# Kernel optimization log

Hardware: AMD Instinct MI355X
Metric: run time of the kernel (lower is better)

The kernel has to match this reference:

```python
import jax, jax.numpy as jnp
import numpy as np

B = 64          # number of scenes/graphs
OBJS = 2048     # objects per scene
N = B * OBJS    # total objects
D = 256         # representation_dim
K = 2           # num_channels


def setup_inputs() -> dict:
    key = jax.random.key(0)
    k1, k2, k3 = jax.random.split(key, 3)
    x_aggregation = jax.random.normal(k1, (N, D), dtype=jnp.float32)
    num_objs = jnp.full((B,), OBJS, dtype=jnp.int32)
    # glorot for att_shared [1, D]: fan_in + fan_out = 1 + D
    std_shared = float(np.sqrt(6.0 / (1 + D)))
    att_shared = jax.random.uniform(k2, (1, D), dtype=jnp.float32,
                                    minval=-std_shared, maxval=std_shared)
    # glorot for att_scale [K, 1]
    std_scale = float(np.sqrt(6.0 / (K + 1)))
    att_scale = jax.random.uniform(k3, (K, 1), dtype=jnp.float32,
                                   minval=-std_scale, maxval=std_scale)
    channel_bias = jnp.zeros((K, D), dtype=jnp.float32)
    return {"x_aggregation": x_aggregation, "num_objs": num_objs,
            "att_shared": att_shared, "att_scale": att_scale,
            "channel_bias": channel_bias}


def reference(x_aggregation, num_objs, att_shared, att_scale, channel_bias):
    batch_idx = jnp.repeat(jnp.arange(B), num_objs, total_repeat_length=N)  # [N]
    # scatter_mean: per-scene context features [B, D]
    seg_sum = jax.ops.segment_sum(x_aggregation, batch_idx, num_segments=B)
    counts = jnp.maximum(num_objs, 1).astype(x_aggregation.dtype)
    ctx = seg_sum / counts[:, None]
    attn_in = jax.nn.leaky_relu(x_aggregation + ctx[batch_idx], negative_slope=0.2)  # [N, D]
    # per-channel logits: ((attn_in + bias[k]) . att_shared) * scale[k]
    base = attn_in @ att_shared[0]                 # [N]
    bias_term = channel_bias @ att_shared[0]       # [K]
    logits = (base[:, None] + bias_term[None, :]) * att_scale[:, 0][None, :]  # [N, K]
    # per-channel segment softmax over objects within each scene
    m = jax.ops.segment_max(logits, batch_idx, num_segments=B)   # [B, K]
    z = jnp.exp(logits - m[batch_idx])
    s = jax.ops.segment_sum(z, batch_idx, num_segments=B)        # [B, K]
    attn_weights = z / s[batch_idx]                              # [N, K]
    # attention-weighted pooling per channel -> [B, D, K]
    weighted = x_aggregation[:, :, None] * attn_weights[:, None, :]  # [N, D, K]
    scene_features = jax.ops.segment_sum(weighted, batch_idx, num_segments=B)
    return scene_features, attn_weights
```

## Files before the change

### kernel.cpp

```cpp
#include <hip/hip_runtime.h>

#define B    64
#define OBJS 2048
#define NTOT (B * OBJS)
#define D    256
#define K    2
#define S1   16
#define CH   (OBJS / S1)
#define RPW  (CH / 4)

#define WS_P1  0
#define WS_UP  (1024 * 256)
#define WS_ZP  (WS_UP + 1024 * 512)
#define WS_E   (WS_ZP + 1024 * 8)

static __device__ __forceinline__ float lrelu02(float v) {
    return v > 0.0f ? v : 0.2f * v;
}

__global__ __launch_bounds__(256) void k1_partial(const float* __restrict__ x,
                                                  float* __restrict__ ws) {
    __shared__ float red[4 * D];
    int blk = blockIdx.x;
    int w = threadIdx.x >> 6, l = threadIdx.x & 63;
    int row0 = blk * CH + w * RPW;

    float4 acc = make_float4(0.f, 0.f, 0.f, 0.f);
    const float* px = x + (size_t)row0 * D + 4 * l;
#pragma unroll 8
    for (int j = 0; j < RPW; ++j) {
        float4 v = *(const float4*)(px + (size_t)j * D);
        acc.x += v.x; acc.y += v.y; acc.z += v.z; acc.w += v.w;
    }
    *(float4*)(red + w * D + 4 * l) = acc;
    __syncthreads();
    int t = threadIdx.x;
    if (t < 64) {
        float4 a = ((const float4*)(red        ))[t];
        float4 e = ((const float4*)(red +     D))[t];
        float4 f = ((const float4*)(red + 2 * D))[t];
        float4 g = ((const float4*)(red + 3 * D))[t];
        float4 s = make_float4(a.x + e.x + f.x + g.x, a.y + e.y + f.y + g.y,
                               a.z + e.z + f.z + g.z, a.w + e.w + f.w + g.w);
        *(float4*)(ws + WS_P1 + blk * D + 4 * t) = s;
    }
}

__global__ __launch_bounds__(256) void k2_main(const float* __restrict__ x,
                                               const int* __restrict__ num_objs,
                                               const float* __restrict__ att_scale,
                                               const float* __restrict__ att_shared,
                                               const float* __restrict__ channel_bias,
                                               float* __restrict__ ws) {
    __shared__ float pl[4 * 576];
    __shared__ float esm[4 * 16];
    __shared__ float sctx[D];
    __shared__ float sbt[2];

    int blk = blockIdx.x;
    int b = blk >> 4;
    int t = threadIdx.x;
    int w = t >> 6, l = t & 63;
    int r = l & 7, s = l >> 3;
    int row0 = blk * CH + w * RPW;

    {
        int cnt = num_objs[b]; if (cnt < 1) cnt = 1;
        float inv = 1.0f / (float)cnt;
        float sum = 0.f;
#pragma unroll
        for (int c = 0; c < S1; ++c) sum += ws[WS_P1 + (b * S1 + c) * D + t];
        sctx[t] = sum * inv;
    }
    if (t < 64) {
        float4 a = ((const float4*)att_shared)[t];
#pragma unroll
        for (int k = 0; k < K; ++k) {
            float4 cb = ((const float4*)(channel_bias + k * D))[t];
            float v = a.x * cb.x + a.y * cb.y + a.z * cb.z + a.w * cb.w;
#pragma unroll
            for (int m = 32; m > 0; m >>= 1) v += __shfl_xor(v, m);
            if (t == 0) sbt[k] = v;
        }
    }
    __syncthreads();

    float4 a4   = ((const float4*)att_shared)[l];
    float4 ctx4 = *(const float4*)(sctx + 4 * l);
    float bt0 = sbt[0], bt1 = sbt[1];
    float s0 = att_scale[0], s1 = att_scale[1];

    float4 acc0 = make_float4(0.f, 0.f, 0.f, 0.f);
    float4 acc1 = make_float4(0.f, 0.f, 0.f, 0.f);
    float z0 = 0.f, z1 = 0.f;
    float e0c = 0.f, e1c = 0.f;
    float* pw = pl  + w * 576;
    float* ew = esm + w * 16;
    const float* px = x + (size_t)row0 * D + 4 * l;

#pragma unroll
    for (int g = 0; g < 4; ++g) {
        float4 v0 = *(const float4*)(px + (size_t)(g * 8 + 0) * D);
        float4 v1 = *(const float4*)(px + (size_t)(g * 8 + 1) * D);
        float4 v2 = *(const float4*)(px + (size_t)(g * 8 + 2) * D);
        float4 v3 = *(const float4*)(px + (size_t)(g * 8 + 3) * D);
        float4 v4 = *(const float4*)(px + (size_t)(g * 8 + 4) * D);
        float4 v5 = *(const float4*)(px + (size_t)(g * 8 + 5) * D);
        float4 v6 = *(const float4*)(px + (size_t)(g * 8 + 6) * D);
        float4 v7 = *(const float4*)(px + (size_t)(g * 8 + 7) * D);

#define PDOT(V) (lrelu02((V).x + ctx4.x) * a4.x + lrelu02((V).y + ctx4.y) * a4.y \
               + lrelu02((V).z + ctx4.z) * a4.z + lrelu02((V).w + ctx4.w) * a4.w)
        pw[l * 9 + 0] = PDOT(v0); pw[l * 9 + 1] = PDOT(v1);
        pw[l * 9 + 2] = PDOT(v2); pw[l * 9 + 3] = PDOT(v3);
        pw[l * 9 + 4] = PDOT(v4); pw[l * 9 + 5] = PDOT(v5);
        pw[l * 9 + 6] = PDOT(v6); pw[l * 9 + 7] = PDOT(v7);
#undef PDOT
        float tr = 0.f;
#pragma unroll
        for (int q = 0; q < 8; ++q) tr += pw[(s * 8 + q) * 9 + r];
        tr += __shfl_xor(tr, 8);
        tr += __shfl_xor(tr, 16);
        tr += __shfl_xor(tr, 32);

        float e0 = __expf((tr + bt0) * s0);
        float e1 = __expf((tr + bt1) * s1);
        if (((l >> 3) & 3) == g) { e0c = e0; e1c = e1; }
        if (l < 8) { ew[2 * l] = e0; ew[2 * l + 1] = e1; }
        float4 E0 = *(const float4*)(ew + 0);
        float4 E1 = *(const float4*)(ew + 4);
        float4 E2 = *(const float4*)(ew + 8);
        float4 E3 = *(const float4*)(ew + 12);
        z0 += E0.x + E0.z + E1.x + E1.z + E2.x + E2.z + E3.x + E3.z;
        z1 += E0.y + E0.w + E1.y + E1.w + E2.y + E2.w + E3.y + E3.w;

#define ACC(V, EA, EB) { acc0.x += (V).x * (EA); acc0.y += (V).y * (EA);      \
                         acc0.z += (V).z * (EA); acc0.w += (V).w * (EA);      \
                         acc1.x += (V).x * (EB); acc1.y += (V).y * (EB);      \
                         acc1.z += (V).z * (EB); acc1.w += (V).w * (EB); }
        ACC(v0, E0.x, E0.y) ACC(v1, E0.z, E0.w)
        ACC(v2, E1.x, E1.y) ACC(v3, E1.z, E1.w)
        ACC(v4, E2.x, E2.y) ACC(v5, E2.z, E2.w)
        ACC(v6, E3.x, E3.y) ACC(v7, E3.z, E3.w)
#undef ACC
    }

    if (l < 32) ((float2*)(ws + WS_E))[row0 + l] = make_float2(e0c, e1c);
    if (l == 0) {
        ws[WS_ZP + blk * 8 + w * 2 + 0] = z0;
        ws[WS_ZP + blk * 8 + w * 2 + 1] = z1;
    }
    __syncthreads();
    {
        int base = w * (D * K) + l * 8;
        pl[base + 0] = acc0.x; pl[base + 1] = acc1.x;
        pl[base + 2] = acc0.y; pl[base + 3] = acc1.y;
        pl[base + 4] = acc0.z; pl[base + 5] = acc1.z;
        pl[base + 6] = acc0.w; pl[base + 7] = acc1.w;
    }
    __syncthreads();
    if (t < 128) {
        float4 a = ((const float4*)(pl       ))[t];
        float4 e = ((const float4*)(pl +  512))[t];
        float4 f = ((const float4*)(pl + 1024))[t];
        float4 g = ((const float4*)(pl + 1536))[t];
        float4 s4 = make_float4(a.x + e.x + f.x + g.x, a.y + e.y + f.y + g.y,
                                a.z + e.z + f.z + g.z, a.w + e.w + f.w + g.w);
        *(float4*)(ws + WS_UP + (size_t)blk * (D * K) + 4 * t) = s4;
    }
}

__global__ __launch_bounds__(256) void k3_final(const float* __restrict__ ws,
                                                float* __restrict__ out) {
    __shared__ float zsh[2];
    int b = blockIdx.x;
    int t = threadIdx.x;
    int w = t >> 6, l = t & 63;

    if (w < 2) {
        float v = ws[WS_ZP + (b * S1 + (l >> 2)) * 8 + (l & 3) * 2 + w];
#pragma unroll
        for (int m = 32; m > 0; m >>= 1) v += __shfl_xor(v, m);
        if (l == 0) zsh[w] = v;
    }
    __syncthreads();
    float z0 = zsh[0], z1 = zsh[1];
    float iz0 = 1.0f / z0, iz1 = 1.0f / z1;

#pragma unroll
    for (int j = t; j < D * K; j += 256) {
        float s = 0.f;
#pragma unroll
        for (int c = 0; c < S1; ++c) s += ws[WS_UP + (b * S1 + c) * (D * K) + j];
        out[b * (D * K) + j] = s * ((j & 1) ? iz1 : iz0);
    }
    const float4* E = (const float4*)(ws + WS_E);
    float4* W = (float4*)(out + B * D * K);
#pragma unroll
    for (int i = t; i < OBJS / 2; i += 256) {
        float4 e = E[b * (OBJS / 2) + i];
        W[b * (OBJS / 2) + i] = make_float4(e.x * iz0, e.y * iz1, e.z * iz0, e.w * iz1);
    }
}

extern "C" void kernel_launch(void* const* d_in, const int* in_sizes, int n_in,
                              void* d_out, int out_size, void* d_ws, size_t ws_size,
                              hipStream_t stream) {
    const float* x            = (const float*)d_in[0];
    const int*   num_objs     = (const int*)d_in[1];
    const float* att_shared   = (const float*)d_in[2];
    const float* att_scale    = (const float*)d_in[3];
    const float* channel_bias = (const float*)d_in[4];
    float* ws  = (float*)d_ws;
    float* out = (float*)d_out;

    k1_partial<<<B * S1, 256, 0, stream>>>(x, ws);
    k2_main<<<B * S1, 256, 0, stream>>>(x, num_objs, att_scale, att_shared,
                                        channel_bias, ws);
    k3_final<<<B, 256, 0, stream>>>(ws, out);
}
```

Measured before the change: 222.7 us.

## Fuse three kernels into one using per-scene atomic barriers

Merges the partial-sum, main and final kernels into one launch. Blocks of a scene meet at an atomic counter barrier to share the context mean, and the last block to arrive does the final normalisation. This removes two kernel launches and the gaps between them, and the second read of x may now hit in cache. In exchange it adds a memset launch and relies on all 16 blocks of a scene being co-resident, which makes the spin-wait a deadlock risk guarded only by an iteration cap.

```diff
diff --git a/kernel.cpp b/kernel.cpp
--- a/kernel.cpp
+++ b/kernel.cpp
@@ -5,57 +5,40 @@
 #define NTOT (B * OBJS)
 #define D    256
 #define K    2
-#define S1   16
-#define CH   (OBJS / S1)
+#define SPB  16
+#define GRID (B * SPB)
+#define CH   (OBJS / SPB)
 #define RPW  (CH / 4)
 
+
 #define WS_P1  0
-#define WS_UP  (1024 * 256)
-#define WS_ZP  (WS_UP + 1024 * 512)
-#define WS_E   (WS_ZP + 1024 * 8)
+#define WS_UP  (GRID * 256)
+#define WS_ZP  (WS_UP + GRID * 512)
+#define WS_E   (WS_ZP + GRID * 8)
+#define WS_CNT (WS_E + NTOT * 2)
 
 static __device__ __forceinline__ float lrelu02(float v) {
     return v > 0.0f ? v : 0.2f * v;
 }
 
-__global__ __launch_bounds__(256) void k1_partial(const float* __restrict__ x,
-                                                  float* __restrict__ ws) {
-    __shared__ float red[4 * D];
-    int blk = blockIdx.x;
-    int w = threadIdx.x >> 6, l = threadIdx.x & 63;
-    int row0 = blk * CH + w * RPW;
-
-    float4 acc = make_float4(0.f, 0.f, 0.f, 0.f);
-    const float* px = x + (size_t)row0 * D + 4 * l;
-#pragma unroll 8
-    for (int j = 0; j < RPW; ++j) {
-        float4 v = *(const float4*)(px + (size_t)j * D);
-        acc.x += v.x; acc.y += v.y; acc.z += v.z; acc.w += v.w;
-    }
-    *(float4*)(red + w * D + 4 * l) = acc;
-    __syncthreads();
-    int t = threadIdx.x;
-    if (t < 64) {
-        float4 a = ((const float4*)(red        ))[t];
-        float4 e = ((const float4*)(red +     D))[t];
-        float4 f = ((const float4*)(red + 2 * D))[t];
-        float4 g = ((const float4*)(red + 3 * D))[t];
-        float4 s = make_float4(a.x + e.x + f.x + g.x, a.y + e.y + f.y + g.y,
-                               a.z + e.z + f.z + g.z, a.w + e.w + f.w + g.w);
-        *(float4*)(ws + WS_P1 + blk * D + 4 * t) = s;
-    }
-}
-
-__global__ __launch_bounds__(256) void k2_main(const float* __restrict__ x,
-                                               const int* __restrict__ num_objs,
-                                               const float* __restrict__ att_scale,
-                                               const float* __restrict__ att_shared,
-                                               const float* __restrict__ channel_bias,
-                                               float* __restrict__ ws) {
+static __device__ __forceinline__ float ldg_agent(const float* p) {
+    return __hip_atomic_load(p, __ATOMIC_RELAXED, __HIP_MEMORY_SCOPE_AGENT);
+}
+
+__global__ __launch_bounds__(256, 4)
+void fused_kernel(const float* __restrict__ x,
+                  const int* __restrict__ num_objs,
+                  const float* __restrict__ att_scale,
+                  const float* __restrict__ att_shared,
+                  const float* __restrict__ channel_bias,
+                  float* __restrict__ ws,
+                  float* __restrict__ out) {
     __shared__ float pl[4 * 576];
     __shared__ float esm[4 * 16];
     __shared__ float sctx[D];
     __shared__ float sbt[2];
+    __shared__ int   sarr;
+    __shared__ float zsh[2];
 
     int blk = blockIdx.x;
     int b = blk >> 4;
@@ -63,25 +46,62 @@
     int w = t >> 6, l = t & 63;
     int r = l & 7, s = l >> 3;
     int row0 = blk * CH + w * RPW;
+    int* cnt1 = (int*)(ws + WS_CNT) + b;
+    int* cnt2 = (int*)(ws + WS_CNT) + 64 + b;
+
+    {
+        float4 acc = make_float4(0.f, 0.f, 0.f, 0.f);
+        const float* px = x + (size_t)row0 * D + 4 * l;
+#pragma unroll 8
+        for (int j = 0; j < RPW; ++j) {
+            float4 v = *(const float4*)(px + (size_t)j * D);
+            acc.x += v.x; acc.y += v.y; acc.z += v.z; acc.w += v.w;
+        }
+        *(float4*)(pl + w * D + 4 * l) = acc;
+    }
+    __syncthreads();
+    if (t < 64) {
+        float4 a = ((const float4*)(pl        ))[t];
+        float4 e = ((const float4*)(pl +     D))[t];
+        float4 f = ((const float4*)(pl + 2 * D))[t];
+        float4 g = ((const float4*)(pl + 3 * D))[t];
+        float4 sm = make_float4(a.x + e.x + f.x + g.x, a.y + e.y + f.y + g.y,
+                                a.z + e.z + f.z + g.z, a.w + e.w + f.w + g.w);
+        *(float4*)(ws + WS_P1 + (size_t)blk * D + 4 * t) = sm;
+    }
+    if (w == 1) {
+        float4 a = ((const float4*)att_shared)[l];
+#pragma unroll
+        for (int k = 0; k < K; ++k) {
+            float4 cb = ((const float4*)(channel_bias + k * D))[l];
+            float v = a.x * cb.x + a.y * cb.y + a.z * cb.z + a.w * cb.w;
+#pragma unroll
+            for (int m = 32; m > 0; m >>= 1) v += __shfl_xor(v, m);
+            if (l == 0) { sbt[0 + k] = v; }
+        }
+    }
+
+    __builtin_amdgcn_fence(__ATOMIC_RELEASE, "agent");
+    __syncthreads();
+    if (t == 0) {
+        __hip_atomic_fetch_add(cnt1, 1, __ATOMIC_ACQ_REL, __HIP_MEMORY_SCOPE_AGENT);
+        int it = 0;
+        while (__hip_atomic_load(cnt1, __ATOMIC_ACQUIRE, __HIP_MEMORY_SCOPE_AGENT) < SPB) {
+            __builtin_amdgcn_s_sleep(2);
+            if (++it > (1 << 24)) break;
+        }
+    }
+    __syncthreads();
+    __builtin_amdgcn_fence(__ATOMIC_ACQUIRE, "agent");
 
     {
         int cnt = num_objs[b]; if (cnt < 1) cnt = 1;
         float inv = 1.0f / (float)cnt;
         float sum = 0.f;
 #pragma unroll
-        for (int c = 0; c < S1; ++c) sum += ws[WS_P1 + (b * S1 + c) * D + t];
+        for (int c = 0; c < SPB; ++c)
+            sum += ldg_agent(&ws[WS_P1 + (size_t)(b * SPB + c) * D + t]);
         sctx[t] = sum * inv;
-    }
-    if (t < 64) {
-        float4 a = ((const float4*)att_shared)[t];
-#pragma unroll
-        for (int k = 0; k < K; ++k) {
-            float4 cb = ((const float4*)(channel_bias + k * D))[t];
-            float v = a.x * cb.x + a.y * cb.y + a.z * cb.z + a.w * cb.w;
-#pragma unroll
-            for (int m = 32; m > 0; m >>= 1) v += __shfl_xor(v, m);
-            if (t == 0) sbt[k] = v;
-        }
     }
     __syncthreads();
 
@@ -168,38 +188,39 @@
                                 a.z + e.z + f.z + g.z, a.w + e.w + f.w + g.w);
         *(float4*)(ws + WS_UP + (size_t)blk * (D * K) + 4 * t) = s4;
     }
-}
-
-__global__ __launch_bounds__(256) void k3_final(const float* __restrict__ ws,
-                                                float* __restrict__ out) {
-    __shared__ float zsh[2];
-    int b = blockIdx.x;
-    int t = threadIdx.x;
-    int w = t >> 6, l = t & 63;
+
+    __builtin_amdgcn_fence(__ATOMIC_RELEASE, "agent");
+    __syncthreads();
+    if (t == 0)
+        sarr = __hip_atomic_fetch_add(cnt2, 1, __ATOMIC_ACQ_REL, __HIP_MEMORY_SCOPE_AGENT);
+    __syncthreads();
+    if (sarr != SPB - 1) return;
+    __builtin_amdgcn_fence(__ATOMIC_ACQUIRE, "agent");
 
     if (w < 2) {
-        float v = ws[WS_ZP + (b * S1 + (l >> 2)) * 8 + (l & 3) * 2 + w];
+        float v = ldg_agent(&ws[WS_ZP + (b * SPB + (l >> 2)) * 8 + (l & 3) * 2 + w]);
 #pragma unroll
         for (int m = 32; m > 0; m >>= 1) v += __shfl_xor(v, m);
         if (l == 0) zsh[w] = v;
     }
     __syncthreads();
-    float z0 = zsh[0], z1 = zsh[1];
-    float iz0 = 1.0f / z0, iz1 = 1.0f / z1;
+    float iz0 = 1.0f / zsh[0], iz1 = 1.0f / zsh[1];
 
 #pragma unroll
     for (int j = t; j < D * K; j += 256) {
-        float s = 0.f;
-#pragma unroll
-        for (int c = 0; c < S1; ++c) s += ws[WS_UP + (b * S1 + c) * (D * K) + j];
-        out[b * (D * K) + j] = s * ((j & 1) ? iz1 : iz0);
+        float sum = 0.f;
+#pragma unroll
+        for (int c = 0; c < SPB; ++c)
+            sum += ldg_agent(&ws[WS_UP + (size_t)(b * SPB + c) * (D * K) + j]);
+        out[b * (D * K) + j] = sum * ((j & 1) ? iz1 : iz0);
     }
     const float4* E = (const float4*)(ws + WS_E);
     float4* W = (float4*)(out + B * D * K);
 #pragma unroll
     for (int i = t; i < OBJS / 2; i += 256) {
-        float4 e = E[b * (OBJS / 2) + i];
-        W[b * (OBJS / 2) + i] = make_float4(e.x * iz0, e.y * iz1, e.z * iz0, e.w * iz1);
+        float4 e4 = E[b * (OBJS / 2) + i];
+        W[b * (OBJS / 2) + i] = make_float4(e4.x * iz0, e4.y * iz1,
+                                            e4.z * iz0, e4.w * iz1);
     }
 }
 
@@ -214,8 +235,9 @@
     float* ws  = (float*)d_ws;
     float* out = (float*)d_out;
 
-    k1_partial<<<B * S1, 256, 0, stream>>>(x, ws);
-    k2_main<<<B * S1, 256, 0, stream>>>(x, num_objs, att_scale, att_shared,
-                                        channel_bias, ws);
-    k3_final<<<B, 256, 0, stream>>>(ws, out);
-}
+    (void)hipMemsetAsync((char*)d_ws + (size_t)WS_CNT * sizeof(float), 0,
+                         128 * sizeof(int), stream);
+
+    fused_kernel<<<GRID, 256, 0, stream>>>(x, num_objs, att_scale, att_shared,
+                                           channel_bias, ws, out);
+}
```

Measured after the change: 653.7 us. 2.94x slower.
